# Kernel tuning notes

Hardware: AMD Instinct MI355X
Metric: run time of the kernel (lower is better)

The kernel has to match this reference:

```python
import math
import jax, jax.numpy as jnp
import numpy as np

HEADS = 16
DIM_HEAD = 64
BSZ = 16        # block_size
EPS = 1e-8


def _flip_every_two(t):
    # t: (B, nblk, z, d) -> flip adjacent pairs along nblk
    B, nblk = t.shape[0], t.shape[1]
    t = t.reshape(B, nblk // 2, 2, *t.shape[2:])
    t = jnp.flip(t, axis=2)
    return t.reshape(B, nblk, *t.shape[3:])


def setup_inputs() -> dict:
    key = jax.random.key(0)
    k1, k2, k3 = jax.random.split(key, 3)
    b, n, dim = 4, 8192, 1024
    inner = HEADS * DIM_HEAD
    x = jax.random.normal(k1, (b, n, dim), dtype=jnp.float32)
    w_qkv = jax.random.normal(k2, (dim, inner * 3), dtype=jnp.float32) * 0.02
    w_out = jax.random.normal(k3, (inner, dim), dtype=jnp.float32) * 0.02
    b_out = jnp.zeros((dim,), dtype=jnp.float32)
    return {"x": x, "w_qkv": w_qkv, "w_out": w_out, "b_out": b_out}


def _hattention(x, w_qkv, w_out, b_out):
    b, n, dim = x.shape  # n assumed power of 2 -> no padding needed
    scale = DIM_HEAD ** -0.5

    qkv = x @ w_qkv                                   # (b, n, 3*inner)
    q, k, v = jnp.split(qkv, 3, axis=-1)

    def to_heads(t):
        return t.reshape(b, n, HEADS, DIM_HEAD).transpose(0, 2, 1, 3).reshape(b * HEADS, n, DIM_HEAD)

    q, k, v = map(to_heads, (q, k, v))
    q = q * scale

    num_levels = int(math.log2(n // BSZ)) - 1

    # build coarsened pyramid: q,k averaged over pairs, v summed
    qkvs = [(q, k, v)]
    for _ in range(num_levels):
        B, m, d = q.shape
        q = q.reshape(B, m // 2, 2, d).mean(axis=2)
        k = k.reshape(B, m // 2, 2, d).mean(axis=2)
        v = v.reshape(B, m // 2, 2, d).sum(axis=2)
        qkvs.append((q, k, v))

    def to_blocks(t):
        return t.reshape(t.shape[0], -1, BSZ, DIM_HEAD)

    Ys = []
    L = len(qkvs)
    for ind, (ql, kl, vl) in enumerate(reversed(qkvs)):
        is_last = ind == L - 1
        qb, kb, vb = map(to_blocks, (ql, kl, vl))
        if not is_last:
            kb = _flip_every_two(kb)
            vb = _flip_every_two(vb)
        # block-local unnormalized softmax attention
        S = jnp.einsum('bnid,bnjd->bnij', qb, kb)
        S = S - jnp.max(S, axis=-1, keepdims=True)
        A = jnp.exp(S)
        y = jnp.einsum('bnij,bnjd->bnid', A, vb)
        Asum = A.sum(axis=-1)
        Ys.append((y.reshape(y.shape[0], -1, DIM_HEAD),
                   Asum.reshape(Asum.shape[0], -1)))

    # combine coarse-to-fine by upsampling (repeat by 2) and summing
    Y, A = Ys[0]
    for Yl, Al in Ys[1:]:
        Y = jnp.repeat(Y, 2, axis=1) + Yl
        A = jnp.repeat(A, 2, axis=1) + Al

    out = Y / (A + EPS)[..., None]                    # (b*h, n, d)
    out = out.reshape(b, HEADS, n, DIM_HEAD).transpose(0, 2, 1, 3).reshape(b, n, HEADS * DIM_HEAD)
    return out @ w_out + b_out


def reference(x, w_qkv, w_out, b_out):
    return _hattention(x, w_qkv, w_out, b_out)
```

## Files before the change

### kernel.cpp

```cpp
#include <hip/hip_runtime.h>
#include <hip/hip_bf16.h>

typedef __bf16 bf16_t;
typedef bf16_t bf16x8 __attribute__((ext_vector_type(8)));
typedef float f32x4 __attribute__((ext_vector_type(4)));

#define PROWS 16352

__device__ __forceinline__ void gl_lds16(const bf16_t* g, bf16_t* l) {
  __builtin_amdgcn_global_load_lds(
      (const __attribute__((address_space(1))) void*)g,
      (__attribute__((address_space(3))) void*)l,
      16, 0, 0);
}

__device__ __forceinline__ void load8f(const bf16_t* p, float* f) {
  bf16x8 v = *(const bf16x8*)p;
#pragma unroll
  for (int e = 0; e < 8; ++e) f[e] = (float)v[e];
}
__device__ __forceinline__ void store8f(bf16_t* p, const float* f) {
  bf16x8 v;
#pragma unroll
  for (int e = 0; e < 8; ++e) v[e] = (bf16_t)f[e];
  *(bf16x8*)p = v;
}

__global__ __launch_bounds__(256) void cvt_f32_to_bf16(const float* __restrict__ in,
                                                       bf16_t* __restrict__ o) {
  size_t gid = (size_t)blockIdx.x * 256 + threadIdx.x;
  const float4* p = (const float4*)in + gid * 2;
  float4 a = p[0], b = p[1];
  bf16x8 v;
  v[0] = (bf16_t)a.x; v[1] = (bf16_t)a.y; v[2] = (bf16_t)a.z; v[3] = (bf16_t)a.w;
  v[4] = (bf16_t)b.x; v[5] = (bf16_t)b.y; v[6] = (bf16_t)b.z; v[7] = (bf16_t)b.w;
  *(bf16x8*)(o + gid * 8) = v;
}

__global__ __launch_bounds__(256) void transpose_to_bf16(const float* __restrict__ w,
                                                         bf16_t* __restrict__ wT,
                                                         int K, int N) {
  __shared__ float t[32][33];
  int bx = blockIdx.x, by = blockIdx.y;
  int tx = threadIdx.x & 31, ty = threadIdx.x >> 5;
#pragma unroll
  for (int r = ty; r < 32; r += 8)
    t[r][tx] = w[(size_t)(by * 32 + r) * N + bx * 32 + tx];
  __syncthreads();
#pragma unroll
  for (int r = ty; r < 32; r += 8)
    wT[(size_t)(bx * 32 + r) * K + by * 32 + tx] = (bf16_t)t[tx][r];
}

template <int EPI>
__global__ __launch_bounds__(512, 2) void gemm256p(const bf16_t* __restrict__ A,
                                                   const bf16_t* __restrict__ Bt,
                                                   float* __restrict__ Cp,
                                                   const float* __restrict__ bias,
                                                   bf16_t* __restrict__ Pq,
                                                   bf16_t* __restrict__ Pk,
                                                   bf16_t* __restrict__ Pv,
                                                   int ldc, int nTilesN, int tilesPerBlock) {
  __shared__ __align__(16) bf16_t As[2 * 256 * 64];
  __shared__ __align__(16) bf16_t Bs[2 * 256 * 64];
  const int LD = 1024;
  const int tid = threadIdx.x;
  const int w = tid >> 6, lane = tid & 63;

  const int chunk = (blockIdx.x & 7) * 32 + (blockIdx.x >> 3);
  const int tile0 = chunk * tilesPerBlock;
  const int nSteps = tilesPerBlock * 16;

  const int wr = w >> 2, wc = w & 3;
  const int lr = lane & 15, lg = lane >> 4;
  const int sw = lr & 7;
  f32x4 acc[8][4] = {};

  auto stageHalf = [&](const bf16_t* __restrict__ G, int rbase, int kt,
                       bf16_t* lbuf, int h) {
#pragma unroll
    for (int j = 0; j < 2; ++j) {
      int b = j * 8 + w;
      int r3 = lane >> 3;
      int k8 = (lane & 7) ^ r3;
      gl_lds16(G + (size_t)(rbase + h * 128 + b * 8 + r3) * LD + kt + k8 * 8,
               lbuf + h * 8192 + b * 512);
    }
  };

  int ntEc = tile0 % nTilesN;
  int bmE = (tile0 / nTilesN) * 256, bnE = ntEc * 256;
  int nt2c = ntEc, bm2 = bmE, bn2 = bnE, kt2 = 128;

  stageHalf(Bt, bnE, 0, Bs, 0); stageHalf(Bt, bnE, 0, Bs, 1);
  stageHalf(A, bmE, 0, As, 0);  stageHalf(A, bmE, 0, As, 1);
  stageHalf(Bt, bnE, 64, Bs + 16384, 0); stageHalf(Bt, bnE, 64, Bs + 16384, 1);
  stageHalf(A, bmE, 64, As + 16384, 0);  stageHalf(A, bmE, 64, As + 16384, 1);
  asm volatile("s_waitcnt vmcnt(8)" ::: "memory");
  __syncthreads();

  for (int g = 0; g < nSteps; ++g) {
    const int c = g & 1;
    bf16_t* Abuf = As + c * 16384;
    bf16_t* Bbuf = Bs + c * 16384;
    const bool pf = (g + 2) < nSteps;
    bf16x8 bfrag[4][2];

#pragma unroll
    for (int p = 0; p < 4; ++p) {
      bf16x8 afrag[2][2];
#pragma unroll
      for (int fi = 0; fi < 2; ++fi)
#pragma unroll
        for (int kk = 0; kk < 2; ++kk)
          afrag[fi][kk] = *(const bf16x8*)&Abuf[(wr * 128 + p * 32 + fi * 16 + lr) * 64 +
                                                (((kk * 4 + lg) ^ sw) * 8)];
      if (p == 0) {
#pragma unroll
        for (int fj = 0; fj < 4; ++fj)
#pragma unroll
          for (int kk = 0; kk < 2; ++kk)
            bfrag[fj][kk] = *(const bf16x8*)&Bbuf[(wc * 64 + fj * 16 + lr) * 64 +
                                                  (((kk * 4 + lg) ^ sw) * 8)];
      }
      if (pf) {
        if (p == 1) stageHalf(Bt, bn2, kt2, Bbuf, 0);
        if (p == 2) stageHalf(Bt, bn2, kt2, Bbuf, 1);
        if (p == 3) { stageHalf(A, bm2, kt2, Abuf, 0); stageHalf(A, bm2, kt2, Abuf, 1); }
      }
      __builtin_amdgcn_s_barrier();
      asm volatile("s_waitcnt lgkmcnt(0)" ::: "memory");
      __builtin_amdgcn_sched_barrier(0);
      __builtin_amdgcn_s_setprio(1);
#pragma unroll
      for (int kk = 0; kk < 2; ++kk)
#pragma unroll
        for (int fi = 0; fi < 2; ++fi)
#pragma unroll
          for (int fj = 0; fj < 4; ++fj)
            acc[p * 2 + fi][fj] = __builtin_amdgcn_mfma_f32_16x16x32_bf16(
                afrag[fi][kk], bfrag[fj][kk], acc[p * 2 + fi][fj], 0, 0, 0);
      __builtin_amdgcn_s_setprio(0);
      if (p == 3) {
        if (pf) asm volatile("s_waitcnt vmcnt(8)" ::: "memory");
        else    asm volatile("s_waitcnt vmcnt(0)" ::: "memory");
      }
      __builtin_amdgcn_s_barrier();
    }

    kt2 += 64;
    if (kt2 == 1024) {
      kt2 = 0; ++nt2c; bn2 += 256;
      if (nt2c == nTilesN) { nt2c = 0; bn2 = 0; bm2 += 256; }
    }

    if ((g & 15) == 15) {
      if (EPI == 1) {
        float bv[4];
#pragma unroll
        for (int fj = 0; fj < 4; ++fj) bv[fj] = bias[bnE + wc * 64 + fj * 16 + lr];
#pragma unroll
        for (int fi = 0; fi < 8; ++fi)
#pragma unroll
          for (int fj = 0; fj < 4; ++fj)
#pragma unroll
            for (int r = 0; r < 4; ++r) {
              int row = bmE + wr * 128 + fi * 16 + lg * 4 + r;
              int col = bnE + wc * 64 + fj * 16 + lr;
              Cp[(size_t)row * ldc + col] = acc[fi][fj][r] + bv[fj];
            }
      } else {
        const int trow0 = (bmE & 8191) + wr * 128 + lg * 4;
        const int hgRow = (bmE >> 13) << 4;
#pragma unroll
        for (int fj = 0; fj < 4; ++fj) {
          int col = bnE + wc * 64 + fj * 16 + lr;
          int tns = col >> 10, col10 = col & 1023;
          int h = col10 >> 6, d = col10 & 63;
          bf16_t* Pt = (tns == 0) ? Pq : (tns == 1 ? Pk : Pv);
          bf16_t* bp = Pt + ((size_t)(hgRow + h) * PROWS + trow0) * 64 + d;
          float scl = (tns == 0) ? 0.125f : 1.f;
#pragma unroll
          for (int fi = 0; fi < 8; ++fi)
#pragma unroll
            for (int r = 0; r < 4; ++r)
              bp[(fi * 16 + r) * 64] = (bf16_t)(acc[fi][fj][r] * scl);
        }
      }
#pragma unroll
      for (int fi = 0; fi < 8; ++fi)
#pragma unroll
        for (int fj = 0; fj < 4; ++fj) acc[fi][fj] = (f32x4){};
      ++ntEc; bnE += 256;
      if (ntEc == nTilesN) { ntEc = 0; bnE = 0; bmE += 256; }
    }
  }
}

__global__ __launch_bounds__(256) void coarsen_lite(bf16_t* __restrict__ Pq,
                                                    bf16_t* __restrict__ Pk,
                                                    bf16_t* __restrict__ Pv) {
  __shared__ float l6s[4][64];
  const int poffA[9] = {0, 8192, 12288, 14336, 15360, 15872, 16128, 16256, 16320};
  const int hg = blockIdx.x >> 5, win = blockIdx.x & 31;
  const int tid = threadIdx.x;
  const int d8 = tid & 7, tb = tid >> 3, wv = tid >> 6;
  const size_t base = (size_t)hg * PROWS;
  const int r0 = win * 256 + tb * 8;

#pragma unroll 1
  for (int tensor = 0; tensor < 3; ++tensor) {
    bf16_t* P = (tensor == 0) ? Pq : (tensor == 1 ? Pk : Pv);
    const bool isv = (tensor == 2);
    float s3[8] = {}, t[8], o[8];
#pragma unroll
    for (int i = 0; i < 8; ++i) {
      load8f(P + (base + r0 + i) * 64 + d8 * 8, t);
#pragma unroll
      for (int e = 0; e < 8; ++e) s3[e] += t[e];
    }
    float s4[8], s5[8], s6[8];
#pragma unroll
    for (int e = 0; e < 8; ++e) s4[e] = s3[e] + __shfl_xor(s3[e], 8, 64);
    if ((tb & 1) == 0) {
      float sc = isv ? 1.f : 0.0625f;
#pragma unroll
      for (int e = 0; e < 8; ++e) o[e] = s4[e] * sc;
      store8f(P + (base + poffA[4] + win * 16 + (tb >> 1)) * 64 + d8 * 8, o);
    }
#pragma unroll
    for (int e = 0; e < 8; ++e) s5[e] = s4[e] + __shfl_xor(s4[e], 16, 64);
    if ((tb & 3) == 0) {
      float sc = isv ? 1.f : 0.03125f;
#pragma unroll
      for (int e = 0; e < 8; ++e) o[e] = s5[e] * sc;
      store8f(P + (base + poffA[5] + win * 8 + (tb >> 2)) * 64 + d8 * 8, o);
    }
#pragma unroll
    for (int e = 0; e < 8; ++e) s6[e] = s5[e] + __shfl_xor(s5[e], 32, 64);
    if ((tb & 7) == 0) {
      float sc = isv ? 1.f : 0.015625f;
#pragma unroll
      for (int e = 0; e < 8; ++e) { o[e] = s6[e] * sc; l6s[wv][d8 * 8 + e] = s6[e]; }
      store8f(P + (base + poffA[6] + win * 4 + wv) * 64 + d8 * 8, o);
    }
    __syncthreads();
    if (tid < 16) {
      int pr = tid >> 3, dd = tid & 7;
      float sc7 = isv ? 1.f : 0.0078125f;
#pragma unroll
      for (int e = 0; e < 8; ++e)
        o[e] = (l6s[2 * pr][dd * 8 + e] + l6s[2 * pr + 1][dd * 8 + e]) * sc7;
      store8f(P + (base + poffA[7] + win * 2 + pr) * 64 + dd * 8, o);
    }
    if (tid < 8) {
      float sc8 = isv ? 1.f : 0.00390625f;
#pragma unroll
      for (int e = 0; e < 8; ++e)
        o[e] = (l6s[0][d8 * 8 + e] + l6s[1][d8 * 8 + e] +
                l6s[2][d8 * 8 + e] + l6s[3][d8 * 8 + e]) * sc8;
      store8f(P + (base + poffA[8] + win) * 64 + d8 * 8, o);
    }
    __syncthreads();
  }
}

__global__ __launch_bounds__(256) void attn_hi(bf16_t* __restrict__ Pq,
                                               const bf16_t* __restrict__ Pk,
                                               const bf16_t* __restrict__ Pv,
                                               float* __restrict__ Asum) {
  const int poffA[9] = {0, 8192, 12288, 14336, 15360, 15872, 16128, 16256, 16320};
  const int tid = threadIdx.x;
  const int wv = tid >> 6, lane = tid & 63;
  const int lr = lane & 15, lg = lane >> 4;

  int bid = blockIdx.x * 4 + wv;
  int l = 4, cnt = 2048;
  while (bid >= cnt) { bid -= cnt; cnt >>= 1; ++l; }
  const int lg2nblk = 9 - l;
  const int blk = bid & ((1 << lg2nblk) - 1);
  const int hg = bid >> lg2nblk;
  const int kvblk = blk ^ 1;
  const size_t qbase = (size_t)hg * PROWS + poffA[l] + blk * 16;
  const size_t kvbase = (size_t)hg * PROWS + poffA[l] + kvblk * 16;

  f32x4 s = {};
#pragma unroll
  for (int c = 0; c < 2; ++c) {
    bf16x8 ak = *(const bf16x8*)(Pk + (kvbase + lr) * 64 + c * 32 + lg * 8);
    bf16x8 bq = *(const bf16x8*)(Pq + (qbase + lr) * 64 + c * 32 + lg * 8);
    s = __builtin_amdgcn_mfma_f32_16x16x32_bf16(ak, bq, s, 0, 0, 0);
  }
  float mx = fmaxf(fmaxf(s[0], s[1]), fmaxf(s[2], s[3]));
  mx = fmaxf(mx, __shfl_xor(mx, 16, 64));
  mx = fmaxf(mx, __shfl_xor(mx, 32, 64));
  float a[4]; float asum = 0.f;
#pragma unroll
  for (int r = 0; r < 4; ++r) { a[r] = (float)(bf16_t)__expf(s[r] - mx); asum += a[r]; }
  asum += __shfl_xor(asum, 16, 64);
  asum += __shfl_xor(asum, 32, 64);
  if (lg == 0) Asum[qbase + lr] = asum;

  const int src0 = (2 * lg) * 16 + lr;
  const int src1 = (2 * lg + 1) * 16 + lr;
  bf16x8 pa;
#pragma unroll
  for (int r = 0; r < 4; ++r) {
    float c0 = __shfl(a[r], src0, 64);
    float c1 = __shfl(a[r], src1, 64);
    pa[r]     = (lg < 2) ? (bf16_t)c0 : (bf16_t)0.f;
    pa[r + 4] = (lg < 2) ? (bf16_t)c1 : (bf16_t)0.f;
  }
#pragma unroll
  for (int dt = 0; dt < 4; ++dt) {
    bf16x8 vf;
    if (lg < 2) {
#pragma unroll
      for (int e = 0; e < 8; ++e) vf[e] = Pv[(kvbase + lg * 8 + e) * 64 + dt * 16 + lr];
    } else {
#pragma unroll
      for (int e = 0; e < 8; ++e) vf[e] = (bf16_t)0.f;
    }
    f32x4 y = __builtin_amdgcn_mfma_f32_16x16x32_bf16(pa, vf, (f32x4){}, 0, 0, 0);
#pragma unroll
    for (int r = 0; r < 4; ++r)
      Pq[(qbase + 4 * lg + r) * 64 + dt * 16 + lr] = (bf16_t)y[r];
  }
}

__global__ __launch_bounds__(256) void attn_comb(const bf16_t* __restrict__ Pq,
                                                 const bf16_t* __restrict__ Pk,
                                                 const bf16_t* __restrict__ Pv,
                                                 const float* __restrict__ Ab,
                                                 bf16_t* __restrict__ attnb) {
  __shared__ __align__(16) bf16_t yl[480 * 72];
  __shared__ float asl[480];
  const int poffA[9] = {0, 8192, 12288, 14336, 15360, 15872, 16128, 16256, 16320};
  const int loffA[4] = {0, 256, 384, 448};
  const int hg = blockIdx.x >> 5, win = blockIdx.x & 31;
  const int tid = threadIdx.x;
  const int wv = tid >> 6, lane = tid & 63;
  const int lr = lane & 15, lg = lane >> 4;
  const size_t hb = (size_t)hg * PROWS;

  auto do_attn = [&](int l, int blkL) {
    const int blk = win * (16 >> l) + blkL;
    const int kvblk = l ? (blk ^ 1) : blk;
    const int lrow = loffA[l] + blkL * 16;
    const int q0 = (blk * 16 + lr) << l;
    const int k0 = (kvblk * 16 + lr) << l;
    const int kv0 = (kvblk * 16) << l;
    const float scl = 1.f / (float)(1 << l);

    f32x4 s = {};
#pragma unroll
    for (int c = 0; c < 2; ++c) {
      float fk[8] = {}, fq[8] = {}, t[8];
      for (int m = 0; m < (1 << l); ++m) {
        load8f(Pk + (hb + k0 + m) * 64 + c * 32 + lg * 8, t);
#pragma unroll
        for (int e = 0; e < 8; ++e) fk[e] += t[e];
        load8f(Pq + (hb + q0 + m) * 64 + c * 32 + lg * 8, t);
#pragma unroll
        for (int e = 0; e < 8; ++e) fq[e] += t[e];
      }
      bf16x8 ak, bq;
#pragma unroll
      for (int e = 0; e < 8; ++e) {
        ak[e] = (bf16_t)(fk[e] * scl);
        bq[e] = (bf16_t)(fq[e] * scl);
      }
      s = __builtin_amdgcn_mfma_f32_16x16x32_bf16(ak, bq, s, 0, 0, 0);
    }

    float mx = fmaxf(fmaxf(s[0], s[1]), fmaxf(s[2], s[3]));
    mx = fmaxf(mx, __shfl_xor(mx, 16, 64));
    mx = fmaxf(mx, __shfl_xor(mx, 32, 64));
    float a[4]; float asum = 0.f;
#pragma unroll
    for (int r = 0; r < 4; ++r) { a[r] = (float)(bf16_t)__expf(s[r] - mx); asum += a[r]; }
    asum += __shfl_xor(asum, 16, 64);
    asum += __shfl_xor(asum, 32, 64);
    if (lg == 0) asl[lrow + lr] = asum;

    if (l == 0) {
      const int src0 = (2 * lg) * 16 + lr;
      const int src1 = (2 * lg + 1) * 16 + lr;
      bf16x8 pa;
#pragma unroll
      for (int r = 0; r < 4; ++r) {
        float c0 = __shfl(a[r], src0, 64);
        float c1 = __shfl(a[r], src1, 64);
        pa[r]     = (lg < 2) ? (bf16_t)c0 : (bf16_t)0.f;
        pa[r + 4] = (lg < 2) ? (bf16_t)c1 : (bf16_t)0.f;
      }
#pragma unroll
      for (int dt = 0; dt < 4; ++dt) {
        bf16x8 vf;
        if (lg < 2) {
#pragma unroll
          for (int e = 0; e < 8; ++e) vf[e] = Pv[(hb + kv0 + lg * 8 + e) * 64 + dt * 16 + lr];
        } else {
#pragma unroll
          for (int e = 0; e < 8; ++e) vf[e] = (bf16_t)0.f;
        }
        f32x4 y = __builtin_amdgcn_mfma_f32_16x16x32_bf16(pa, vf, (f32x4){}, 0, 0, 0);
#pragma unroll
        for (int r = 0; r < 4; ++r)
          yl[(lrow + 4 * lg + r) * 72 + dt * 16 + lr] = (bf16_t)y[r];
      }
    } else {
      const int nch = 1 << (l - 1);
      bf16x8 pa[4];
      for (int ch = 0; ch < nch; ++ch) {
        if (l == 1) {
#pragma unroll
          for (int e = 0; e < 8; ++e) pa[ch][e] = (bf16_t)a[e >> 1];
        } else if (l == 2) {
          int src = (2 * ch + (lg >> 1)) * 16 + lr;
          float t0 = __shfl(a[0], src, 64), t1 = __shfl(a[1], src, 64);
          float t2 = __shfl(a[2], src, 64), t3 = __shfl(a[3], src, 64);
          float vlo = (lg & 1) ? t2 : t0;
          float vhi = (lg & 1) ? t3 : t1;
#pragma unroll
          for (int e = 0; e < 4; ++e) { pa[ch][e] = (bf16_t)vlo; pa[ch][e + 4] = (bf16_t)vhi; }
        } else {
          int src = ch * 16 + lr;
          float t0 = __shfl(a[0], src, 64), t1 = __shfl(a[1], src, 64);
          float t2 = __shfl(a[2], src, 64), t3 = __shfl(a[3], src, 64);
          float v01 = (lg & 1) ? t1 : t0;
          float v23 = (lg & 1) ? t3 : t2;
          float vv = (lg & 2) ? v23 : v01;
#pragma unroll
          for (int e = 0; e < 8; ++e) pa[ch][e] = (bf16_t)vv;
        }
      }
#pragma unroll
      for (int dt = 0; dt < 4; ++dt) {
        f32x4 y = {};
        for (int ch = 0; ch < nch; ++ch) {
          bf16x8 vf;
#pragma unroll
          for (int e = 0; e < 8; ++e)
            vf[e] = Pv[(hb + kv0 + ch * 32 + lg * 8 + e) * 64 + dt * 16 + lr];
          y = __builtin_amdgcn_mfma_f32_16x16x32_bf16(pa[ch], vf, y, 0, 0, 0);
        }
#pragma unroll
        for (int r = 0; r < 4; ++r)
          yl[(lrow + 4 * lg + r) * 72 + dt * 16 + lr] = (bf16_t)y[r];
      }
    }
  };

  do_attn(0, wv * 4 + 0); do_attn(0, wv * 4 + 1);
  do_attn(0, wv * 4 + 2); do_attn(0, wv * 4 + 3);
  do_attn(1, wv * 2 + 0); do_attn(1, wv * 2 + 1);
  do_attn(2, wv);
  if (wv < 2) do_attn(3, wv);
  __syncthreads();

  const int d8 = tid & 7, rg = tid >> 3;
#pragma unroll
  for (int i = 0; i < 8; ++i) {
    const int r = rg * 8 + i;
    const int t = win * 256 + r;
    float acc[8] = {};
    float asum = 0.f;
#pragma unroll
    for (int l = 0; l < 4; ++l) {
      const int row = loffA[l] + (r >> l);
      asum += asl[row];
      bf16x8 v = *(const bf16x8*)&yl[row * 72 + d8 * 8];
#pragma unroll
      for (int e = 0; e < 8; ++e) acc[e] += (float)v[e];
    }
#pragma unroll
    for (int l = 4; l < 9; ++l) {
      const size_t grow = hb + poffA[l] + (t >> l);
      asum += Ab[grow];
      bf16x8 v = *(const bf16x8*)(Pq + grow * 64 + d8 * 8);
#pragma unroll
      for (int e = 0; e < 8; ++e) acc[e] += (float)v[e];
    }
    const float inv = 1.f / (asum + 1e-8f);
    bf16x8 o;
#pragma unroll
    for (int e = 0; e < 8; ++e) o[e] = (bf16_t)(acc[e] * inv);
    *(bf16x8*)(attnb + ((size_t)(hg >> 4) * 8192 + t) * 1024 + (hg & 15) * 64 + d8 * 8) = o;
  }
}

extern "C" void kernel_launch(void* const* d_in, const int* in_sizes, int n_in,
                              void* d_out, int out_size, void* d_ws, size_t ws_size,
                              hipStream_t stream) {
  const float* x = (const float*)d_in[0];
  const float* wqkv = (const float*)d_in[1];
  const float* wout = (const float*)d_in[2];
  const float* bout = (const float*)d_in[3];
  float* out = (float*)d_out;
  (void)in_sizes; (void)n_in; (void)out_size; (void)ws_size;

  char* base = (char*)d_ws;
  bf16_t* Pq    = (bf16_t*)(base + 0);
  bf16_t* Pk    = (bf16_t*)(base + 133955584);
  bf16_t* Pv    = (bf16_t*)(base + 267911168);
  float*  Ab    = (float*)(base + 401866752);
  bf16_t* woutT = (bf16_t*)(base + 406052864);
  bf16_t* x_bf  = (bf16_t*)(base + 408150016);
  bf16_t* wqkvT = (bf16_t*)(base + 475258880);
  bf16_t* attnb = (bf16_t*)(base + 408150016);

  cvt_f32_to_bf16<<<16384, 256, 0, stream>>>(x, x_bf);
  transpose_to_bf16<<<dim3(96, 32), 256, 0, stream>>>(wqkv, wqkvT, 1024, 3072);
  transpose_to_bf16<<<dim3(32, 32), 256, 0, stream>>>(wout, woutT, 1024, 1024);

  gemm256p<0><<<256, 512, 0, stream>>>(x_bf, wqkvT, nullptr, nullptr, Pq, Pk, Pv,
                                       3072, 12, 6);

  coarsen_lite<<<2048, 256, 0, stream>>>(Pq, Pk, Pv);

  attn_hi<<<992, 256, 0, stream>>>(Pq, Pk, Pv, Ab);
  attn_comb<<<2048, 256, 0, stream>>>(Pq, Pk, Pv, Ab, attnb);

  gemm256p<1><<<256, 512, 0, stream>>>(attnb, woutT, out, bout, nullptr, nullptr, nullptr,
                                       1024, 4, 2);
}
```

Before: 550.1 us.

## Replace persistent 256x256 GEMM with one-tile-per-block 128x128 double-buffered GEMM

Both projection GEMMs move from a persistent 512-thread kernel that walks several 256x256 tiles per block with a cross-tile prefetch pipeline to a simple 256-thread kernel where each block computes a single 128x128 tile. The grid is launched with many more blocks (6144 and 2048), and the K loop double-buffers 64-wide slices with one barrier pair per step. This trades the larger tile's operand reuse and the finer-grained phase interleaving for more blocks, higher occupancy and simpler scheduling. Each output element now needs its operands staged from global memory twice as often, which raises LDS and L2 traffic.

```diff
diff --git a/kernel.cpp b/kernel.cpp
--- a/kernel.cpp
+++ b/kernel.cpp
@@ -53,146 +53,115 @@
 }
 
 template <int EPI>
-__global__ __launch_bounds__(512, 2) void gemm256p(const bf16_t* __restrict__ A,
-                                                   const bf16_t* __restrict__ Bt,
-                                                   float* __restrict__ Cp,
-                                                   const float* __restrict__ bias,
-                                                   bf16_t* __restrict__ Pq,
-                                                   bf16_t* __restrict__ Pk,
-                                                   bf16_t* __restrict__ Pv,
-                                                   int ldc, int nTilesN, int tilesPerBlock) {
-  __shared__ __align__(16) bf16_t As[2 * 256 * 64];
-  __shared__ __align__(16) bf16_t Bs[2 * 256 * 64];
-  const int LD = 1024;
+__global__ __launch_bounds__(256) void gemm128d(const bf16_t* __restrict__ A,
+                                                const bf16_t* __restrict__ Bt,
+                                                float* __restrict__ Cp,
+                                                const float* __restrict__ bias,
+                                                bf16_t* __restrict__ Pq,
+                                                bf16_t* __restrict__ Pk,
+                                                bf16_t* __restrict__ Pv,
+                                                int ldc, int nTilesN) {
+  __shared__ __align__(16) bf16_t As[2 * 128 * 64];
+  __shared__ __align__(16) bf16_t Bs[2 * 128 * 64];
   const int tid = threadIdx.x;
   const int w = tid >> 6, lane = tid & 63;
 
-  const int chunk = (blockIdx.x & 7) * 32 + (blockIdx.x >> 3);
-  const int tile0 = chunk * tilesPerBlock;
-  const int nSteps = tilesPerBlock * 16;
-
-  const int wr = w >> 2, wc = w & 3;
+  const int nwg = gridDim.x;
+  const int chunk = (blockIdx.x & 7) * (nwg >> 3) + (blockIdx.x >> 3);
+  const int mt = chunk / nTilesN, ntile = chunk % nTilesN;
+  const int bm = mt * 128, bn = ntile * 128;
+
+  const int wr = w >> 1, wc = w & 1;
   const int lr = lane & 15, lg = lane >> 4;
   const int sw = lr & 7;
-  f32x4 acc[8][4] = {};
-
-  auto stageHalf = [&](const bf16_t* __restrict__ G, int rbase, int kt,
-                       bf16_t* lbuf, int h) {
-#pragma unroll
-    for (int j = 0; j < 2; ++j) {
-      int b = j * 8 + w;
+  f32x4 acc[4][4] = {};
+
+  auto stageMat = [&](const bf16_t* __restrict__ G, int rbase, int kt,
+                      bf16_t* lbuf) {
+#pragma unroll
+    for (int j = 0; j < 4; ++j) {
+      int b = j * 4 + w;
       int r3 = lane >> 3;
       int k8 = (lane & 7) ^ r3;
-      gl_lds16(G + (size_t)(rbase + h * 128 + b * 8 + r3) * LD + kt + k8 * 8,
-               lbuf + h * 8192 + b * 512);
+      gl_lds16(G + (size_t)(rbase + b * 8 + r3) * 1024 + kt + k8 * 8,
+               lbuf + b * 512);
     }
   };
 
-  int ntEc = tile0 % nTilesN;
-  int bmE = (tile0 / nTilesN) * 256, bnE = ntEc * 256;
-  int nt2c = ntEc, bm2 = bmE, bn2 = bnE, kt2 = 128;
-
-  stageHalf(Bt, bnE, 0, Bs, 0); stageHalf(Bt, bnE, 0, Bs, 1);
-  stageHalf(A, bmE, 0, As, 0);  stageHalf(A, bmE, 0, As, 1);
-  stageHalf(Bt, bnE, 64, Bs + 16384, 0); stageHalf(Bt, bnE, 64, Bs + 16384, 1);
-  stageHalf(A, bmE, 64, As + 16384, 0);  stageHalf(A, bmE, 64, As + 16384, 1);
-  asm volatile("s_waitcnt vmcnt(8)" ::: "memory");
-  __syncthreads();
-
-  for (int g = 0; g < nSteps; ++g) {
-    const int c = g & 1;
-    bf16_t* Abuf = As + c * 16384;
-    bf16_t* Bbuf = Bs + c * 16384;
-    const bool pf = (g + 2) < nSteps;
-    bf16x8 bfrag[4][2];
-
-#pragma unroll
-    for (int p = 0; p < 4; ++p) {
-      bf16x8 afrag[2][2];
-#pragma unroll
-      for (int fi = 0; fi < 2; ++fi)
-#pragma unroll
-        for (int kk = 0; kk < 2; ++kk)
-          afrag[fi][kk] = *(const bf16x8*)&Abuf[(wr * 128 + p * 32 + fi * 16 + lr) * 64 +
-                                                (((kk * 4 + lg) ^ sw) * 8)];
-      if (p == 0) {
+  stageMat(A, bm, 0, As);
+  stageMat(Bt, bn, 0, Bs);
+
+  for (int t = 0; t < 16; ++t) {
+    const int c = t & 1;
+    bf16_t* Ac = As + c * 8192;
+    bf16_t* Bc = Bs + c * 8192;
+    if (t < 15) {
+      const int kt1 = (t + 1) << 6;
+      stageMat(A, bm, kt1, As + (c ^ 1) * 8192);
+      stageMat(Bt, bn, kt1, Bs + (c ^ 1) * 8192);
+      asm volatile("s_waitcnt vmcnt(8)" ::: "memory");
+    } else {
+      asm volatile("s_waitcnt vmcnt(0)" ::: "memory");
+    }
+    __builtin_amdgcn_s_barrier();
+
+    bf16x8 af[4][2], bfv[4][2];
+#pragma unroll
+    for (int fi = 0; fi < 4; ++fi)
+#pragma unroll
+      for (int kk = 0; kk < 2; ++kk)
+        af[fi][kk] = *(const bf16x8*)&Ac[(wr * 64 + fi * 16 + lr) * 64 +
+                                         (((kk * 4 + lg) ^ sw) * 8)];
+#pragma unroll
+    for (int fj = 0; fj < 4; ++fj)
+#pragma unroll
+      for (int kk = 0; kk < 2; ++kk)
+        bfv[fj][kk] = *(const bf16x8*)&Bc[(wc * 64 + fj * 16 + lr) * 64 +
+                                          (((kk * 4 + lg) ^ sw) * 8)];
+#pragma unroll
+    for (int kk = 0; kk < 2; ++kk)
+#pragma unroll
+      for (int fi = 0; fi < 4; ++fi)
 #pragma unroll
         for (int fj = 0; fj < 4; ++fj)
-#pragma unroll
-          for (int kk = 0; kk < 2; ++kk)
-            bfrag[fj][kk] = *(const bf16x8*)&Bbuf[(wc * 64 + fj * 16 + lr) * 64 +
-                                                  (((kk * 4 + lg) ^ sw) * 8)];
-      }
-      if (pf) {
-        if (p == 1) stageHalf(Bt, bn2, kt2, Bbuf, 0);
-        if (p == 2) stageHalf(Bt, bn2, kt2, Bbuf, 1);
-        if (p == 3) { stageHalf(A, bm2, kt2, Abuf, 0); stageHalf(A, bm2, kt2, Abuf, 1); }
-      }
-      __builtin_amdgcn_s_barrier();
-      asm volatile("s_waitcnt lgkmcnt(0)" ::: "memory");
-      __builtin_amdgcn_sched_barrier(0);
-      __builtin_amdgcn_s_setprio(1);
-#pragma unroll
-      for (int kk = 0; kk < 2; ++kk)
-#pragma unroll
-        for (int fi = 0; fi < 2; ++fi)
-#pragma unroll
-          for (int fj = 0; fj < 4; ++fj)
-            acc[p * 2 + fi][fj] = __builtin_amdgcn_mfma_f32_16x16x32_bf16(
-                afrag[fi][kk], bfrag[fj][kk], acc[p * 2 + fi][fj], 0, 0, 0);
-      __builtin_amdgcn_s_setprio(0);
-      if (p == 3) {
-        if (pf) asm volatile("s_waitcnt vmcnt(8)" ::: "memory");
-        else    asm volatile("s_waitcnt vmcnt(0)" ::: "memory");
-      }
-      __builtin_amdgcn_s_barrier();
-    }
-
-    kt2 += 64;
-    if (kt2 == 1024) {
-      kt2 = 0; ++nt2c; bn2 += 256;
-      if (nt2c == nTilesN) { nt2c = 0; bn2 = 0; bm2 += 256; }
-    }
-
-    if ((g & 15) == 15) {
-      if (EPI == 1) {
-        float bv[4];
-#pragma unroll
-        for (int fj = 0; fj < 4; ++fj) bv[fj] = bias[bnE + wc * 64 + fj * 16 + lr];
-#pragma unroll
-        for (int fi = 0; fi < 8; ++fi)
-#pragma unroll
-          for (int fj = 0; fj < 4; ++fj)
-#pragma unroll
-            for (int r = 0; r < 4; ++r) {
-              int row = bmE + wr * 128 + fi * 16 + lg * 4 + r;
-              int col = bnE + wc * 64 + fj * 16 + lr;
-              Cp[(size_t)row * ldc + col] = acc[fi][fj][r] + bv[fj];
-            }
-      } else {
-        const int trow0 = (bmE & 8191) + wr * 128 + lg * 4;
-        const int hgRow = (bmE >> 13) << 4;
-#pragma unroll
-        for (int fj = 0; fj < 4; ++fj) {
-          int col = bnE + wc * 64 + fj * 16 + lr;
-          int tns = col >> 10, col10 = col & 1023;
-          int h = col10 >> 6, d = col10 & 63;
-          bf16_t* Pt = (tns == 0) ? Pq : (tns == 1 ? Pk : Pv);
-          bf16_t* bp = Pt + ((size_t)(hgRow + h) * PROWS + trow0) * 64 + d;
-          float scl = (tns == 0) ? 0.125f : 1.f;
-#pragma unroll
-          for (int fi = 0; fi < 8; ++fi)
-#pragma unroll
-            for (int r = 0; r < 4; ++r)
-              bp[(fi * 16 + r) * 64] = (bf16_t)(acc[fi][fj][r] * scl);
+          acc[fi][fj] = __builtin_amdgcn_mfma_f32_16x16x32_bf16(
+              af[fi][kk], bfv[fj][kk], acc[fi][fj], 0, 0, 0);
+
+    asm volatile("s_waitcnt lgkmcnt(0)" ::: "memory");
+    __builtin_amdgcn_sched_barrier(0);
+    __builtin_amdgcn_s_barrier();
+  }
+
+  if (EPI == 1) {
+    float bv[4];
+#pragma unroll
+    for (int fj = 0; fj < 4; ++fj) bv[fj] = bias[bn + wc * 64 + fj * 16 + lr];
+#pragma unroll
+    for (int fi = 0; fi < 4; ++fi)
+#pragma unroll
+      for (int fj = 0; fj < 4; ++fj)
+#pragma unroll
+        for (int r = 0; r < 4; ++r) {
+          int row = bm + wr * 64 + fi * 16 + lg * 4 + r;
+          int col = bn + wc * 64 + fj * 16 + lr;
+          Cp[(size_t)row * ldc + col] = acc[fi][fj][r] + bv[fj];
         }
-      }
-#pragma unroll
-      for (int fi = 0; fi < 8; ++fi)
-#pragma unroll
-        for (int fj = 0; fj < 4; ++fj) acc[fi][fj] = (f32x4){};
-      ++ntEc; bnE += 256;
-      if (ntEc == nTilesN) { ntEc = 0; bnE = 0; bmE += 256; }
+  } else {
+    const int trow0 = (bm & 8191) + wr * 64 + lg * 4;
+    const int hgRow = (bm >> 13) << 4;
+#pragma unroll
+    for (int fj = 0; fj < 4; ++fj) {
+      int col = bn + wc * 64 + fj * 16 + lr;
+      int tns = col >> 10, col10 = col & 1023;
+      int h = col10 >> 6, d = col10 & 63;
+      bf16_t* Pt = (tns == 0) ? Pq : (tns == 1 ? Pk : Pv);
+      bf16_t* bp = Pt + ((size_t)(hgRow + h) * PROWS + trow0) * 64 + d;
+      float scl = (tns == 0) ? 0.125f : 1.f;
+#pragma unroll
+      for (int fi = 0; fi < 4; ++fi)
+#pragma unroll
+        for (int r = 0; r < 4; ++r)
+          bp[(fi * 16 + r) * 64] = (bf16_t)(acc[fi][fj][r] * scl);
     }
   }
 }
@@ -514,14 +483,14 @@
   transpose_to_bf16<<<dim3(96, 32), 256, 0, stream>>>(wqkv, wqkvT, 1024, 3072);
   transpose_to_bf16<<<dim3(32, 32), 256, 0, stream>>>(wout, woutT, 1024, 1024);
 
-  gemm256p<0><<<256, 512, 0, stream>>>(x_bf, wqkvT, nullptr, nullptr, Pq, Pk, Pv,
-                                       3072, 12, 6);
+  gemm128d<0><<<6144, 256, 0, stream>>>(x_bf, wqkvT, nullptr, nullptr, Pq, Pk, Pv,
+                                        3072, 24);
 
   coarsen_lite<<<2048, 256, 0, stream>>>(Pq, Pk, Pv);
 
   attn_hi<<<992, 256, 0, stream>>>(Pq, Pk, Pv, Ab);
   attn_comb<<<2048, 256, 0, stream>>>(Pq, Pk, Pv, Ab, attnb);
 
-  gemm256p<1><<<256, 512, 0, stream>>>(attnb, woutT, out, bout, nullptr, nullptr, nullptr,
-                                       1024, 4, 2);
-}
+  gemm128d<1><<<2048, 256, 0, stream>>>(attnb, woutT, out, bout, nullptr, nullptr, nullptr,
+                                        1024, 8);
+}
```

Measured after the change: 607.5 us. +10.4%, slower.

## Replace persistent multi-tile GEMM with one-tile-per-block grid and LDS-staged QKV epilogue

Applied to the files above, without the earlier changes.

Replaces the persistent GEMM, where each of 256 blocks walked several output tiles with cross-tile prefetch, with a plain launch of one 256x256 tile per workgroup (1536 and 512 blocks) using an XCD-aware block remap. The QKV epilogue now stages bf16 results through LDS with padded rows and writes 16-byte vectors to the head-major layout, instead of scattered 2-byte stores. This trades away cross-tile prefetch overlap for simpler scheduling and more blocks in flight, and it makes the global stores coalesced.

```diff
diff --git a/kernel.cpp b/kernel.cpp
--- a/kernel.cpp
+++ b/kernel.cpp
@@ -53,57 +53,61 @@
 }
 
 template <int EPI>
-__global__ __launch_bounds__(512, 2) void gemm256p(const bf16_t* __restrict__ A,
-                                                   const bf16_t* __restrict__ Bt,
-                                                   float* __restrict__ Cp,
-                                                   const float* __restrict__ bias,
-                                                   bf16_t* __restrict__ Pq,
-                                                   bf16_t* __restrict__ Pk,
-                                                   bf16_t* __restrict__ Pv,
-                                                   int ldc, int nTilesN, int tilesPerBlock) {
+__global__ __launch_bounds__(512, 2) void gemm256(const bf16_t* __restrict__ A,
+                                                  const bf16_t* __restrict__ Bt,
+                                                  float* __restrict__ Cp,
+                                                  const float* __restrict__ bias,
+                                                  bf16_t* __restrict__ Pq,
+                                                  bf16_t* __restrict__ Pk,
+                                                  bf16_t* __restrict__ Pv,
+                                                  int K, int ldc, int nTilesN) {
   __shared__ __align__(16) bf16_t As[2 * 256 * 64];
   __shared__ __align__(16) bf16_t Bs[2 * 256 * 64];
-  const int LD = 1024;
   const int tid = threadIdx.x;
   const int w = tid >> 6, lane = tid & 63;
 
-  const int chunk = (blockIdx.x & 7) * 32 + (blockIdx.x >> 3);
-  const int tile0 = chunk * tilesPerBlock;
-  const int nSteps = tilesPerBlock * 16;
+  int nwg = gridDim.x;
+  int chunk = nwg >> 3;
+  int wgid = (blockIdx.x & 7) * chunk + (blockIdx.x >> 3);
+  int mt = wgid / nTilesN, ntile = wgid % nTilesN;
+  const int bm = mt * 256, bn = ntile * 256;
 
   const int wr = w >> 2, wc = w & 3;
   const int lr = lane & 15, lg = lane >> 4;
   const int sw = lr & 7;
+  const int nt = K >> 6;
+
   f32x4 acc[8][4] = {};
 
-  auto stageHalf = [&](const bf16_t* __restrict__ G, int rbase, int kt,
+  auto stageHalf = [&](const bf16_t* __restrict__ G, int rbase, int kt, int ld,
                        bf16_t* lbuf, int h) {
 #pragma unroll
     for (int j = 0; j < 2; ++j) {
       int b = j * 8 + w;
       int r3 = lane >> 3;
       int k8 = (lane & 7) ^ r3;
-      gl_lds16(G + (size_t)(rbase + h * 128 + b * 8 + r3) * LD + kt + k8 * 8,
+      gl_lds16(G + (size_t)(rbase + h * 128 + b * 8 + r3) * ld + kt + k8 * 8,
                lbuf + h * 8192 + b * 512);
     }
   };
 
-  int ntEc = tile0 % nTilesN;
-  int bmE = (tile0 / nTilesN) * 256, bnE = ntEc * 256;
-  int nt2c = ntEc, bm2 = bmE, bn2 = bnE, kt2 = 128;
-
-  stageHalf(Bt, bnE, 0, Bs, 0); stageHalf(Bt, bnE, 0, Bs, 1);
-  stageHalf(A, bmE, 0, As, 0);  stageHalf(A, bmE, 0, As, 1);
-  stageHalf(Bt, bnE, 64, Bs + 16384, 0); stageHalf(Bt, bnE, 64, Bs + 16384, 1);
-  stageHalf(A, bmE, 64, As + 16384, 0);  stageHalf(A, bmE, 64, As + 16384, 1);
-  asm volatile("s_waitcnt vmcnt(8)" ::: "memory");
+  stageHalf(Bt, bn, 0, K, Bs, 0); stageHalf(Bt, bn, 0, K, Bs, 1);
+  stageHalf(A, bm, 0, K, As, 0);  stageHalf(A, bm, 0, K, As, 1);
+  if (nt > 1) {
+    stageHalf(Bt, bn, 64, K, Bs + 16384, 0); stageHalf(Bt, bn, 64, K, Bs + 16384, 1);
+    stageHalf(A, bm, 64, K, As + 16384, 0);  stageHalf(A, bm, 64, K, As + 16384, 1);
+    asm volatile("s_waitcnt vmcnt(8)" ::: "memory");
+  } else {
+    asm volatile("s_waitcnt vmcnt(0)" ::: "memory");
+  }
   __syncthreads();
 
-  for (int g = 0; g < nSteps; ++g) {
-    const int c = g & 1;
+  for (int t = 0; t < nt; ++t) {
+    const int c = t & 1;
     bf16_t* Abuf = As + c * 16384;
     bf16_t* Bbuf = Bs + c * 16384;
-    const bool pf = (g + 2) < nSteps;
+    const bool pf = (t + 2) < nt;
+    const int kt2 = (t + 2) << 6;
     bf16x8 bfrag[4][2];
 
 #pragma unroll
@@ -124,9 +128,9 @@
                                                   (((kk * 4 + lg) ^ sw) * 8)];
       }
       if (pf) {
-        if (p == 1) stageHalf(Bt, bn2, kt2, Bbuf, 0);
-        if (p == 2) stageHalf(Bt, bn2, kt2, Bbuf, 1);
-        if (p == 3) { stageHalf(A, bm2, kt2, Abuf, 0); stageHalf(A, bm2, kt2, Abuf, 1); }
+        if (p == 1) stageHalf(Bt, bn, kt2, K, Bbuf, 0);
+        if (p == 2) stageHalf(Bt, bn, kt2, K, Bbuf, 1);
+        if (p == 3) { stageHalf(A, bm, kt2, K, Abuf, 0); stageHalf(A, bm, kt2, K, Abuf, 1); }
       }
       __builtin_amdgcn_s_barrier();
       asm volatile("s_waitcnt lgkmcnt(0)" ::: "memory");
@@ -147,52 +151,51 @@
       }
       __builtin_amdgcn_s_barrier();
     }
-
-    kt2 += 64;
-    if (kt2 == 1024) {
-      kt2 = 0; ++nt2c; bn2 += 256;
-      if (nt2c == nTilesN) { nt2c = 0; bn2 = 0; bm2 += 256; }
-    }
-
-    if ((g & 15) == 15) {
-      if (EPI == 1) {
-        float bv[4];
-#pragma unroll
-        for (int fj = 0; fj < 4; ++fj) bv[fj] = bias[bnE + wc * 64 + fj * 16 + lr];
-#pragma unroll
-        for (int fi = 0; fi < 8; ++fi)
-#pragma unroll
-          for (int fj = 0; fj < 4; ++fj)
-#pragma unroll
-            for (int r = 0; r < 4; ++r) {
-              int row = bmE + wr * 128 + fi * 16 + lg * 4 + r;
-              int col = bnE + wc * 64 + fj * 16 + lr;
-              Cp[(size_t)row * ldc + col] = acc[fi][fj][r] + bv[fj];
-            }
-      } else {
-        const int trow0 = (bmE & 8191) + wr * 128 + lg * 4;
-        const int hgRow = (bmE >> 13) << 4;
-#pragma unroll
-        for (int fj = 0; fj < 4; ++fj) {
-          int col = bnE + wc * 64 + fj * 16 + lr;
-          int tns = col >> 10, col10 = col & 1023;
-          int h = col10 >> 6, d = col10 & 63;
-          bf16_t* Pt = (tns == 0) ? Pq : (tns == 1 ? Pk : Pv);
-          bf16_t* bp = Pt + ((size_t)(hgRow + h) * PROWS + trow0) * 64 + d;
-          float scl = (tns == 0) ? 0.125f : 1.f;
-#pragma unroll
-          for (int fi = 0; fi < 8; ++fi)
-#pragma unroll
-            for (int r = 0; r < 4; ++r)
-              bp[(fi * 16 + r) * 64] = (bf16_t)(acc[fi][fj][r] * scl);
+  }
+
+  if (EPI == 1) {
+    float bv[4];
+#pragma unroll
+    for (int fj = 0; fj < 4; ++fj) bv[fj] = bias[bn + wc * 64 + fj * 16 + lr];
+#pragma unroll
+    for (int fi = 0; fi < 8; ++fi)
+#pragma unroll
+      for (int fj = 0; fj < 4; ++fj)
+#pragma unroll
+        for (int r = 0; r < 4; ++r) {
+          int row = bm + wr * 128 + fi * 16 + lg * 4 + r;
+          int col = bn + wc * 64 + fj * 16 + lr;
+          Cp[(size_t)row * ldc + col] = acc[fi][fj][r] + bv[fj];
         }
-      }
-#pragma unroll
-      for (int fi = 0; fi < 8; ++fi)
-#pragma unroll
-        for (int fj = 0; fj < 4; ++fj) acc[fi][fj] = (f32x4){};
-      ++ntEc; bnE += 256;
-      if (ntEc == nTilesN) { ntEc = 0; bnE = 0; bmE += 256; }
+  } else {
+    const int tns = bn >> 10;
+    const int h = ((bn & 1023) >> 6) + wc;
+    const int hgRow = (bm >> 13) << 4;
+    const int trow0 = (bm & 8191) + wr * 128;
+    bf16_t* Pt = (tns == 0) ? Pq : (tns == 1 ? Pk : Pv);
+    const float scl = (tns == 0) ? 0.125f : 1.f;
+    bf16_t* lds = (w < 4) ? (As + w * 4608) : (Bs + (w - 4) * 4608);
+    const size_t gbase = ((size_t)(hgRow + h) * PROWS + trow0) * 64;
+#pragma unroll
+    for (int half = 0; half < 2; ++half) {
+#pragma unroll
+      for (int fi4 = 0; fi4 < 4; ++fi4) {
+        const int fi = half * 4 + fi4;
+#pragma unroll
+        for (int fj = 0; fj < 4; ++fj)
+#pragma unroll
+          for (int r = 0; r < 4; ++r)
+            lds[(fi4 * 16 + lg * 4 + r) * 72 + fj * 16 + lr] =
+                (bf16_t)(acc[fi][fj][r] * scl);
+      }
+      asm volatile("s_waitcnt lgkmcnt(0)" ::: "memory");
+#pragma unroll
+      for (int it = 0; it < 8; ++it) {
+        const int row = it * 8 + (lane >> 3);
+        bf16x8 v = *(const bf16x8*)&lds[row * 72 + (lane & 7) * 8];
+        *(bf16x8*)(Pt + gbase + (size_t)(half * 64 + row) * 64 + (lane & 7) * 8) = v;
+      }
+      asm volatile("s_waitcnt lgkmcnt(0)" ::: "memory");
     }
   }
 }
@@ -514,14 +517,14 @@
   transpose_to_bf16<<<dim3(96, 32), 256, 0, stream>>>(wqkv, wqkvT, 1024, 3072);
   transpose_to_bf16<<<dim3(32, 32), 256, 0, stream>>>(wout, woutT, 1024, 1024);
 
-  gemm256p<0><<<256, 512, 0, stream>>>(x_bf, wqkvT, nullptr, nullptr, Pq, Pk, Pv,
-                                       3072, 12, 6);
+  gemm256<0><<<1536, 512, 0, stream>>>(x_bf, wqkvT, nullptr, nullptr, Pq, Pk, Pv,
+                                       1024, 3072, 12);
 
   coarsen_lite<<<2048, 256, 0, stream>>>(Pq, Pk, Pv);
 
   attn_hi<<<992, 256, 0, stream>>>(Pq, Pk, Pv, Ab);
   attn_comb<<<2048, 256, 0, stream>>>(Pq, Pk, Pv, Ab, attnb);
 
-  gemm256p<1><<<256, 512, 0, stream>>>(attnb, woutT, out, bout, nullptr, nullptr, nullptr,
-                                       1024, 4, 2);
-}
+  gemm256<1><<<512, 512, 0, stream>>>(attnb, woutT, out, bout, nullptr, nullptr, nullptr,
+                                      1024, 1024, 4);
+}
```

Result: no change. 542.5 us (-1.4%).
